# Optimization experiments

Measured on AMD Instinct MI355X. Metric: run time of the kernel, lower is better.

## Reference

```python
import jax, jax.numpy as jnp
import numpy as np
from jax import lax

EPS = 1e-6

def rms_norm(x, w):
    return x * lax.rsqrt(jnp.mean(x * x, axis=-1, keepdims=True) + EPS) * w

def rec_layer(x, conv_w, conv_b, Wr_w, Wr_b, Wi_w, Wi_b, log_a, out_w, norm_w):
    # x: [B, L, d]; depthwise causal conv, kernel size 4
    B, L, d = x.shape
    xc = lax.conv_general_dilated(
        x.transpose(0, 2, 1), conv_w, window_strides=(1,), padding=[(3, 0)],
        dimension_numbers=("NCH", "OIH", "NCH"), feature_group_count=d)
    x_conv = xc.transpose(0, 2, 1) + conv_b  # [B, L, d]
    r_t = jax.nn.sigmoid(x_conv @ Wr_w.T + Wr_b)
    i_t = jax.nn.sigmoid(x_conv @ Wi_w.T + Wi_b)
    a_base = jax.nn.sigmoid(log_a)  # [d]
    a_t = jnp.power(a_base, 8.0 * r_t)  # [B, L, d]
    u_t = i_t * x_conv

    def step(h, au):
        a, u = au
        h = a * h + jnp.sqrt(jnp.clip(1.0 - a * a, 0.0, None)) * u
        return h, h

    _, hs = lax.scan(step, jnp.zeros((B, d), x.dtype),
                     (a_t.transpose(1, 0, 2), u_t.transpose(1, 0, 2)))
    out = hs.transpose(1, 0, 2)  # [B, L, d]
    return rms_norm(out @ out_w.T, norm_w)

def setup_inputs() -> dict:
    B, L, M, d, do = 8, 2048, 256, 1024, 256
    key = jax.random.key(0)
    ks = jax.random.split(key, 24)
    inp = {
        "concept_out": jax.random.normal(ks[0], (B, M, d), jnp.float32),
        "encoder_out": jax.random.normal(ks[1], (B, L, d), jnp.float32),
        "boundary_probs": jax.random.uniform(ks[2], (B, L), jnp.float32),
        "boundary_idx": jnp.sort(jax.random.randint(ks[3], (B, M), 0, L, jnp.int32), axis=1),
        "gate_w": jax.random.normal(ks[4], (d, d), jnp.float32) * 0.02,
        "gate_b": jnp.zeros((d,), jnp.float32),
        "down_w": jax.random.normal(ks[5], (do, d), jnp.float32) * 0.02,
        "up_w": jax.random.normal(ks[6], (d, do), jnp.float32) * 0.02,
        "norm_out_w": jnp.ones((d,), jnp.float32),
        "rec_conv_w": jax.random.normal(ks[7], (3, do, 1, 4), jnp.float32) * 0.02,
        "rec_conv_b": jnp.zeros((3, do), jnp.float32),
        "rec_Wr_w": jax.random.normal(ks[8], (3, do, do), jnp.float32) * 0.02,
        "rec_Wr_b": jnp.zeros((3, do), jnp.float32),
        "rec_Wi_w": jax.random.normal(ks[9], (3, do, do), jnp.float32) * 0.02,
        "rec_Wi_b": jnp.zeros((3, do), jnp.float32),
        "rec_log_a": jnp.full((3, do), 7.5, jnp.float32),
        "rec_out_w": jax.random.normal(ks[10], (3, do, do), jnp.float32) * 0.02,
        "rec_norm_w": jnp.ones((3, do), jnp.float32),
    }
    return inp

def reference(concept_out, encoder_out, boundary_probs, boundary_idx,
              gate_w, gate_b, down_w, up_w, norm_out_w,
              rec_conv_w, rec_conv_b, rec_Wr_w, rec_Wr_b,
              rec_Wi_w, rec_Wi_b, rec_log_a, rec_out_w, rec_norm_w):
    B, L, d = encoder_out.shape
    M = concept_out.shape[1]
    # 1. EMA smoothing over boundaries
    p_at_bounds = jnp.take_along_axis(boundary_probs, boundary_idx, axis=1)  # [B, M]

    def ema_step(h, pc):
        p_i, c_i = pc  # [B], [B, d]
        h = p_i[:, None] * c_i + (1.0 - p_i[:, None]) * h
        return h, h

    _, sm = lax.scan(ema_step, jnp.zeros((B, d), concept_out.dtype),
                     (p_at_bounds.T, concept_out.transpose(1, 0, 2)))
    smoothed = sm.transpose(1, 0, 2)  # [B, M, d]
    # 2. Plug-back via searchsorted (== torch.bucketize right=True)
    arange_L = jnp.arange(L)
    counts = jax.vmap(lambda bi: jnp.searchsorted(bi, arange_L, side="right"))(boundary_idx)
    bucket = jnp.clip(counts - 1, 0, None)  # [B, L]
    plugback = jnp.take_along_axis(smoothed, bucket[..., None], axis=1)  # [B, L, d]
    # 3. Gated residual
    gate = jax.nn.sigmoid(encoder_out @ gate_w.T + gate_b)
    h = (1.0 - boundary_probs[..., None]) * gate * encoder_out + plugback
    # 4. Decoder recurrence
    h = h @ down_w.T
    for k in range(3):
        h = rec_layer(h, rec_conv_w[k], rec_conv_b[k], rec_Wr_w[k], rec_Wr_b[k],
                      rec_Wi_w[k], rec_Wi_b[k], rec_log_a[k], rec_out_w[k], rec_norm_w[k])
    h = h @ up_w.T
    return rms_norm(h, norm_out_w)
```

## Files before the change

kernel.cpp:

```cpp
#include <hip/hip_runtime.h>
#include <hip/hip_bf16.h>
#include <stdint.h>

typedef __attribute__((ext_vector_type(8))) short short8;
typedef __attribute__((ext_vector_type(4))) float f32x4;
typedef __hip_bfloat16 bf16;

#define NB   8
#define LSEQ 2048
#define NM   256
#define DMODEL 1024
#define DO   256
#define BLR  16384
#define NCH  32
#define CLK  64

__device__ __forceinline__ float sigm(float x) { return 1.f / (1.f + __expf(-x)); }

__device__ __forceinline__ void gl_lds16(const void* g, void* l) {
  __builtin_amdgcn_global_load_lds((const __attribute__((address_space(1))) void*)g,
                                   (__attribute__((address_space(3))) void*)l, 16, 0, 0);
}

__device__ __forceinline__ short8 ds_read128(const bf16* p) {
  short8 r;
  unsigned a = (unsigned)(uintptr_t)(const __attribute__((address_space(3))) bf16*)p;
  asm volatile("ds_read_b128 %0, %1" : "=v"(r) : "v"(a));
  return r;
}

__device__ __forceinline__ unsigned short bf16bits(float v) {
  bf16 b = __float2bfloat16(v);
  return *(unsigned short*)&b;
}
__device__ __forceinline__ float bits2f(unsigned short u) {
  bf16 b = *(bf16*)&u;
  return __bfloat162float(b);
}


__global__ __launch_bounds__(256) void prep_kernel(
    const float* __restrict__ gate_w, const float* __restrict__ down_w,
    const float* __restrict__ up_w, const float* __restrict__ wr_w,
    const float* __restrict__ wi_w, const float* __restrict__ ow_w,
    const float* __restrict__ log_a,
    bf16* __restrict__ gate_wb, bf16* __restrict__ down_wb, bf16* __restrict__ up_wb,
    bf16* __restrict__ wrb, bf16* __restrict__ wib, bf16* __restrict__ owb,
    float* __restrict__ e8) {
  int i = blockIdx.x * 256 + threadIdx.x;
  if (i < 1048576) { gate_wb[i] = __float2bfloat16(gate_w[i]); return; }
  i -= 1048576;
  if (i < 262144) { down_wb[i] = __float2bfloat16(down_w[i]); return; }
  i -= 262144;
  if (i < 262144) { up_wb[i] = __float2bfloat16(up_w[i]); return; }
  i -= 262144;
  if (i < 196608) { wrb[i] = __float2bfloat16(wr_w[i]); return; }
  i -= 196608;
  if (i < 196608) { wib[i] = __float2bfloat16(wi_w[i]); return; }
  i -= 196608;
  if (i < 196608) { owb[i] = __float2bfloat16(ow_w[i]); return; }
  i -= 196608;
  if (i < 768) {
    float ab = 1.f / (1.f + expf(-log_a[i]));
    e8[i] = 8.f * log2f(ab);
  }
}

__global__ __launch_bounds__(256) void cvt4_kernel(const float4* __restrict__ in,
                                                   ushort4* __restrict__ out, int n4) {
  int i = blockIdx.x * 256 + threadIdx.x;
  if (i < n4) {
    float4 v = in[i];
    ushort4 o;
    o.x = bf16bits(v.x); o.y = bf16bits(v.y); o.z = bf16bits(v.z); o.w = bf16bits(v.w);
    out[i] = o;
  }
}


__global__ __launch_bounds__(256) void ema_kernel(const float* __restrict__ cpt,
                                                  const float* __restrict__ bprobs,
                                                  const int* __restrict__ bidx,
                                                  float* __restrict__ smoothed) {
  int b = blockIdx.x >> 2;
  int c = ((blockIdx.x & 3) << 8) + threadIdx.x;
  __shared__ float p[NM];
  p[threadIdx.x] = bprobs[b * LSEQ + bidx[b * NM + threadIdx.x]];
  __syncthreads();
  const float* cp = cpt + (size_t)b * NM * DMODEL + c;
  float* sp = smoothed + (size_t)b * NM * DMODEL + c;
  float h = 0.f;
  for (int m = 0; m < NM; ++m) {
    float pm = p[m];
    h = pm * cp[(size_t)m * DMODEL] + (1.f - pm) * h;
    sp[(size_t)m * DMODEL] = h;
  }
}

__global__ __launch_bounds__(256) void bucket_kernel(const int* __restrict__ bidx,
                                                     int* __restrict__ bucket) {
  int i = blockIdx.x * 256 + threadIdx.x;
  int b = i >> 11, l = i & 2047;
  const int* bi = bidx + b * NM;
  int lo = 0, hi = NM;
  while (lo < hi) {
    int mid = (lo + hi) >> 1;
    if (bi[mid] <= l) lo = mid + 1; else hi = mid;
  }
  int v = lo - 1;
  bucket[i] = v < 0 ? 0 : v;
}


__global__ __launch_bounds__(256) void gate_plug_kernel(bf16* __restrict__ h0,
                                                        const bf16* __restrict__ encb,
                                                        const float* __restrict__ gbias,
                                                        const float* __restrict__ bprobs,
                                                        const int* __restrict__ bucket,
                                                        const float* __restrict__ smoothed) {
  const int m = blockIdx.x;
  const int t = threadIdx.x;
  const int b = m >> 11;
  const float pm1 = 1.f - bprobs[m];
  const float* srow = smoothed + ((size_t)(b * NM + bucket[m])) * DMODEL + t * 4;
  const size_t base = (size_t)m * DMODEL + t * 4;
  ushort4 gr = *(const ushort4*)(h0 + base);
  ushort4 er = *(const ushort4*)(encb + base);
  float4 sm4 = *(const float4*)srow;
  float4 gb4 = *(const float4*)(gbias + t * 4);
  ushort4 o;
  o.x = bf16bits(pm1 * sigm(bits2f(gr.x) + gb4.x) * bits2f(er.x) + sm4.x);
  o.y = bf16bits(pm1 * sigm(bits2f(gr.y) + gb4.y) * bits2f(er.y) + sm4.y);
  o.z = bf16bits(pm1 * sigm(bits2f(gr.z) + gb4.z) * bits2f(er.z) + sm4.z);
  o.w = bf16bits(pm1 * sigm(bits2f(gr.w) + gb4.w) * bits2f(er.w) + sm4.w);
  *(ushort4*)(h0 + base) = o;
}


__global__ __launch_bounds__(256) void conv_kernel(const bf16* __restrict__ x,
                                                   const float* __restrict__ cw,
                                                   const float* __restrict__ cb,
                                                   bf16* __restrict__ xcb) {
  int i = blockIdx.x * 256 + threadIdx.x;
  int c = i & 255;
  int bl = i >> 8;
  int l = bl & 2047;
  float4 w4 = ((const float4*)cw)[c];
  const float* wf = (const float*)&w4;
  float s = cb[c];
#pragma unroll
  for (int kk = 0; kk < 4; ++kk) {
    int ll = l - 3 + kk;
    if (ll >= 0) s += wf[kk] * __bfloat162float(x[i + (kk - 3) * 256]);
  }
  xcb[i] = __float2bfloat16(s);
}


__global__ __launch_bounds__(256) void scan_p1(const unsigned int* __restrict__ ds,
                                               float2* __restrict__ AS) {
  int b = blockIdx.x >> 5, ch = blockIdx.x & 31, c = threadIdx.x;
  size_t base = ((size_t)b * LSEQ + ch * CLK) * DO + c;
  float A = 1.f, S = 0.f;
  for (int t = 0; t < CLK; ++t) {
    unsigned int u = ds[base + (size_t)t * DO];
    float d = bits2f((unsigned short)(u & 0xffff));
    float s = bits2f((unsigned short)(u >> 16));
    float a = 1.f - d;
    A *= a;
    S = __builtin_fmaf(a, S, s);
  }
  AS[blockIdx.x * DO + c] = make_float2(A, S);
}

__global__ __launch_bounds__(256) void scan_p2(const unsigned int* __restrict__ ds,
                                               const float2* __restrict__ AS,
                                               bf16* __restrict__ hs) {
  int b = blockIdx.x >> 5, ch = blockIdx.x & 31, c = threadIdx.x;
  float h = 0.f;
  for (int j = 0; j < ch; ++j) {
    float2 as = AS[(b * NCH + j) * DO + c];
    h = __builtin_fmaf(as.x, h, as.y);
  }
  size_t base = ((size_t)b * LSEQ + ch * CLK) * DO + c;
  for (int t = 0; t < CLK; ++t) {
    unsigned int u = ds[base + (size_t)t * DO];
    float d = bits2f((unsigned short)(u & 0xffff));
    float s = bits2f((unsigned short)(u >> 16));
    h = __builtin_fmaf(-d, h, h) + s;
    hs[base + (size_t)t * DO] = __float2bfloat16(h);
  }
}


__global__ __launch_bounds__(256) void rmsnorm1024_kernel(const bf16* __restrict__ in,
                                                          const float* __restrict__ w,
                                                          float* __restrict__ out) {
  int row = blockIdx.x, t = threadIdx.x;
  ushort4 raw = ((const ushort4*)(in + (size_t)row * 1024))[t];
  float v0 = bits2f(raw.x), v1 = bits2f(raw.y), v2 = bits2f(raw.z), v3 = bits2f(raw.w);
  float ss = v0 * v0 + v1 * v1 + v2 * v2 + v3 * v3;
#pragma unroll
  for (int ofs = 32; ofs > 0; ofs >>= 1) ss += __shfl_down(ss, ofs, 64);
  __shared__ float wsum[4];
  if ((t & 63) == 0) wsum[t >> 6] = ss;
  __syncthreads();
  float tot = wsum[0] + wsum[1] + wsum[2] + wsum[3];
  float sc = rsqrtf(tot * (1.f / 1024.f) + 1e-6f);
  float4 wv = ((const float4*)w)[t];
  float4 o;
  o.x = v0 * sc * wv.x; o.y = v1 * sc * wv.y;
  o.z = v2 * sc * wv.z; o.w = v3 * sc * wv.w;
  ((float4*)(out + (size_t)row * 1024))[t] = o;
}


struct EpA {
  bf16* outb;
  const float* bias;
  const bf16* encb;
  const float* p;
  const int* bucket;
  const float* smoothed;
};


template <int EP, int NC, int KC>
__global__ __launch_bounds__(256) void gemm_bt(const bf16* __restrict__ A,
                                               const bf16* __restrict__ W, EpA ep) {
  __shared__ __align__(16) bf16 As[128 * 64];
  __shared__ __align__(16) bf16 Bs[128 * 64];
  const int t = threadIdx.x;
  const int lane = t & 63;
  const int wv = t >> 6;
  const int wm = wv >> 1, wn = wv & 1;
  const int quad = lane >> 4, l16 = lane & 15;
  const int bm = blockIdx.x << 7, bn = blockIdx.y << 7;

  f32x4 acc[4][4] = {};

  for (int k0 = 0; k0 < KC; k0 += 64) {
    __syncthreads();
#pragma unroll
    for (int i = 0; i < 4; ++i) {
      int slot = i * 256 + t;
      int m = slot >> 3;
      int lk8 = (slot & 7) ^ (m & 7);
      gl_lds16(A + (size_t)(bm + m) * KC + k0 + lk8 * 8, As + slot * 8);
      gl_lds16(W + (size_t)(bn + m) * KC + k0 + lk8 * 8, Bs + slot * 8);
    }
    __syncthreads();
#pragma unroll
    for (int ks = 0; ks < 2; ++ks) {
      short8 af[4], bfr[4];
#pragma unroll
      for (int i = 0; i < 4; ++i) {
        int m = wm * 64 + i * 16 + l16;
        int pa = (ks * 4 + quad) ^ (m & 7);
        af[i] = *(const short8*)(As + m * 64 + pa * 8);
        int n = wn * 64 + i * 16 + l16;
        int pb = (ks * 4 + quad) ^ (n & 7);
        bfr[i] = *(const short8*)(Bs + n * 64 + pb * 8);
      }
#pragma unroll
      for (int i = 0; i < 4; ++i)
#pragma unroll
        for (int j = 0; j < 4; ++j)
          acc[i][j] = __builtin_amdgcn_mfma_f32_16x16x32_bf16(af[i], bfr[j], acc[i][j], 0, 0, 0);
    }
  }

#pragma unroll
  for (int i = 0; i < 4; ++i) {
#pragma unroll
    for (int j = 0; j < 4; ++j) {
#pragma unroll
      for (int r = 0; r < 4; ++r) {
        int m = bm + wm * 64 + i * 16 + quad * 4 + r;
        int n = bn + wn * 64 + j * 16 + l16;
        size_t idx = (size_t)m * NC + n;
        float v = acc[i][j][r];
        if (EP == 1) {
          float g = sigm(v + ep.bias[n]);
          float pm = ep.p[m];
          int bb = m >> 11;
          float sm = ep.smoothed[((size_t)(bb * NM + ep.bucket[m])) * DMODEL + n];
          float e = __bfloat162float(ep.encb[idx]);
          ep.outb[idx] = __float2bfloat16((1.f - pm) * g * e + sm);
        } else {
          ep.outb[idx] = __float2bfloat16(v);
        }
      }
    }
  }
}


template <int KC>
__global__ __launch_bounds__(512, 2) void gemm256(const bf16* __restrict__ Ag,
                                                  const bf16* __restrict__ W,
                                                  bf16* __restrict__ outb) {
  __shared__ __align__(16) bf16 lds[2][4][128 * 64];
  const int t = threadIdx.x;
  const int lane = t & 63;
  const int wv = t >> 6;
  const int wm = wv >> 2, wn = wv & 3;
  const int quad = lane >> 4, l16 = lane & 15;
  const int bm = blockIdx.x << 8, bn = blockIdx.y << 8;
  constexpr int KT = KC >> 6;
  constexpr int KM = KT - 1;

  const int rr = t >> 3;
  const int cc = (t & 7) ^ (rr & 7);

  f32x4 acc[8][4] = {};
  short8 af[4][2], bfr[2][2];

#define STAGE_A(BUF, H, KTI)                                                      \
  {                                                                               \
    int kk = ((KTI) & KM) << 6;                                                   \
    const bf16* s0 = Ag + (size_t)(bm + (H) * 64 + rr) * KC + kk + cc * 8;        \
    gl_lds16(s0, &lds[BUF][H][t * 8]);                                            \
    const bf16* s1 = Ag + (size_t)(bm + (H) * 64 + rr + 128) * KC + kk + cc * 8;  \
    gl_lds16(s1, &lds[BUF][H][(512 + t) * 8]);                                    \
  }
#define STAGE_B(BUF, H, KTI)                                                      \
  {                                                                               \
    int kk = ((KTI) & KM) << 6;                                                   \
    int n0 = (H) * 32 + (rr & 31) + ((rr >> 5) << 6);                             \
    const bf16* s0 = W + (size_t)(bn + n0) * KC + kk + cc * 8;                    \
    gl_lds16(s0, &lds[BUF][2 + (H)][t * 8]);                                      \
    const bf16* s1 = W + (size_t)(bn + n0 + 128) * KC + kk + cc * 8;              \
    gl_lds16(s1, &lds[BUF][2 + (H)][(512 + t) * 8]);                              \
  }
#define LD_A(BUF, MG)                                                             \
  _Pragma("unroll") for (int ii = 0; ii < 4; ++ii) {                              \
    int r = wm * 64 + ii * 16 + l16;                                              \
    _Pragma("unroll") for (int ks = 0; ks < 2; ++ks) {                            \
      int ch = (ks * 4 + quad) ^ (r & 7);                                         \
      af[ii][ks] = ds_read128(&lds[BUF][MG][(r * 8 + ch) * 8]);                   \
    }                                                                             \
  }
#define LD_B(BUF, NG)                                                             \
  _Pragma("unroll") for (int jj = 0; jj < 2; ++jj) {                              \
    int r = wn * 32 + jj * 16 + l16;                                              \
    _Pragma("unroll") for (int ks = 0; ks < 2; ++ks) {                            \
      int ch = (ks * 4 + quad) ^ (r & 7);                                         \
      bfr[jj][ks] = ds_read128(&lds[BUF][2 + (NG)][(r * 8 + ch) * 8]);            \
    }                                                                             \
  }
#define MMA(MG, NG)                                                               \
  _Pragma("unroll") for (int ks = 0; ks < 2; ++ks)                                \
  _Pragma("unroll") for (int ii = 0; ii < 4; ++ii)                                \
  _Pragma("unroll") for (int jj = 0; jj < 2; ++jj)                                \
    acc[(MG) * 4 + ii][(NG) * 2 + jj] = __builtin_amdgcn_mfma_f32_16x16x32_bf16(  \
        af[ii][ks], bfr[jj][ks], acc[(MG) * 4 + ii][(NG) * 2 + jj], 0, 0, 0);
#define BARR __builtin_amdgcn_s_barrier()
#define WAIT_LGKM asm volatile("s_waitcnt lgkmcnt(0)" ::: "memory")
#define WAIT_VM6 asm volatile("s_waitcnt vmcnt(6)" ::: "memory")
#define SBAR __builtin_amdgcn_sched_barrier(0)
#define PH(MG, NG)                   \
  BARR; WAIT_LGKM; SBAR;             \
  __builtin_amdgcn_s_setprio(1);     \
  MMA(MG, NG);                       \
  __builtin_amdgcn_s_setprio(0);     \
  SBAR;                              \
  BARR;
#define PH_V(MG, NG)                 \
  BARR; WAIT_LGKM; SBAR;             \
  __builtin_amdgcn_s_setprio(1);     \
  MMA(MG, NG);                       \
  __builtin_amdgcn_s_setprio(0);     \
  SBAR;                              \
  WAIT_VM6;                          \
  BARR;

  STAGE_A(0, 0, 0) STAGE_A(0, 1, 0) STAGE_B(0, 0, 0) STAGE_B(0, 1, 0)
  STAGE_A(1, 0, 1) STAGE_A(1, 1, 1) STAGE_B(1, 1, 1)
  WAIT_VM6;
  BARR;

#pragma unroll 1
  for (int it = 0; it < (KT >> 1); ++it) {
    const int kt = it * 2;
    LD_A(0, 0) LD_B(0, 0)
    STAGE_B(1, 0, kt + 1)
    PH(0, 0)
    LD_B(0, 1)
    STAGE_A(0, 0, kt + 2)
    PH(0, 1)
    LD_A(0, 1)
    STAGE_B(0, 1, kt + 2)
    PH(1, 1)
    LD_B(0, 0)
    STAGE_A(0, 1, kt + 2)
    PH_V(1, 0)
    LD_A(1, 0) LD_B(1, 0)
    STAGE_B(0, 0, kt + 2)
    PH(0, 0)
    LD_B(1, 1)
    STAGE_A(1, 0, kt + 3)
    PH(0, 1)
    LD_A(1, 1)
    STAGE_B(1, 1, kt + 3)
    PH(1, 1)
    LD_B(1, 0)
    STAGE_A(1, 1, kt + 3)
    PH_V(1, 0)
  }

#undef STAGE_A
#undef STAGE_B
#undef LD_A
#undef LD_B
#undef MMA
#undef BARR
#undef WAIT_LGKM
#undef WAIT_VM6
#undef SBAR
#undef PH
#undef PH_V

#pragma unroll
  for (int i = 0; i < 8; ++i) {
#pragma unroll
    for (int j = 0; j < 4; ++j) {
#pragma unroll
      for (int r = 0; r < 4; ++r) {
        int m = bm + wm * 128 + i * 16 + quad * 4 + r;
        int n = bn + wn * 64 + j * 16 + l16;
        outb[(size_t)m * DMODEL + n] = __float2bfloat16(acc[i][j][r]);
      }
    }
  }
}


__global__ __launch_bounds__(256, 4) void gemm_ri(const bf16* __restrict__ A,
                                                  const bf16* __restrict__ Wr,
                                                  const bf16* __restrict__ Wi,
                                                  const float* __restrict__ rbias,
                                                  const float* __restrict__ ibias,
                                                  const float* __restrict__ e8,
                                                  unsigned int* __restrict__ ds_out) {
  __shared__ __align__(16) bf16 As[32 * 64];
  __shared__ __align__(16) bf16 Br[128 * 64];
  __shared__ __align__(16) bf16 Bi[128 * 64];
  const int t = threadIdx.x;
  const int lane = t & 63;
  const int wv = t >> 6;
  const int wm = wv >> 1, wn = wv & 1;
  const int quad = lane >> 4, l16 = lane & 15;
  const int bm = blockIdx.x << 5;
  const int bn = blockIdx.y << 7;

  f32x4 ar[4] = {};
  f32x4 ai[4] = {};

  for (int k0 = 0; k0 < DO; k0 += 64) {
    __syncthreads();
    {
      int m = t >> 3, lk8 = (t & 7) ^ (m & 7);
      gl_lds16(A + (size_t)(bm + m) * DO + k0 + lk8 * 8, As + t * 8);
    }
#pragma unroll
    for (int i = 0; i < 4; ++i) {
      int slot = i * 256 + t;
      int n = slot >> 3, lk8 = (slot & 7) ^ (n & 7);
      gl_lds16(Wr + (size_t)(bn + n) * DO + k0 + lk8 * 8, Br + slot * 8);
      gl_lds16(Wi + (size_t)(bn + n) * DO + k0 + lk8 * 8, Bi + slot * 8);
    }
    __syncthreads();
#pragma unroll
    for (int ks = 0; ks < 2; ++ks) {
      int m = wm * 16 + l16;
      int pa = (ks * 4 + quad) ^ (m & 7);
      short8 af = *(const short8*)(As + m * 64 + pa * 8);
#pragma unroll
      for (int j = 0; j < 4; ++j) {
        int n = wn * 64 + j * 16 + l16;
        int pb = (ks * 4 + quad) ^ (n & 7);
        short8 br = *(const short8*)(Br + n * 64 + pb * 8);
        short8 bi = *(const short8*)(Bi + n * 64 + pb * 8);
        ar[j] = __builtin_amdgcn_mfma_f32_16x16x32_bf16(af, br, ar[j], 0, 0, 0);
        ai[j] = __builtin_amdgcn_mfma_f32_16x16x32_bf16(af, bi, ai[j], 0, 0, 0);
      }
    }
  }

#pragma unroll
  for (int j = 0; j < 4; ++j) {
    int n = bn + wn * 64 + j * 16 + l16;
    float rb = rbias[n], ib = ibias[n], e8n = e8[n];
#pragma unroll
    for (int r = 0; r < 4; ++r) {
      int m = bm + wm * 16 + quad * 4 + r;
      size_t idx = (size_t)m * DO + n;
      float rv = sigm(ar[j][r] + rb);
      float a = exp2f(rv * e8n);
      float d = 1.f - a;
      float iv = sigm(ai[j][r] + ib);
      float xc = __bfloat162float(A[idx]);
      float s = sqrtf(fmaxf(1.f - a * a, 0.f)) * iv * xc;
      ds_out[idx] = (unsigned int)bf16bits(d) | ((unsigned int)bf16bits(s) << 16);
    }
  }
}


__global__ __launch_bounds__(256) void gemm_on(const bf16* __restrict__ A,
                                               const bf16* __restrict__ W,
                                               const float* __restrict__ rnw,
                                               bf16* __restrict__ xb) {
  __shared__ __align__(16) bf16 As[64 * 64];
  __shared__ __align__(16) bf16 Bs[256 * 64];
  __shared__ float red[4][64];
  const int t = threadIdx.x;
  const int lane = t & 63;
  const int wn = t >> 6;
  const int quad = lane >> 4, l16 = lane & 15;
  const int bm = blockIdx.x << 6;

  f32x4 acc[4][4] = {};

  for (int k0 = 0; k0 < DO; k0 += 64) {
    __syncthreads();
#pragma unroll
    for (int i = 0; i < 2; ++i) {
      int slot = i * 256 + t;
      int m = slot >> 3;
      int lk8 = (slot & 7) ^ (m & 7);
      gl_lds16(A + (size_t)(bm + m) * DO + k0 + lk8 * 8, As + slot * 8);
    }
#pragma unroll
    for (int i = 0; i < 8; ++i) {
      int slot = i * 256 + t;
      int n = slot >> 3;
      int lk8 = (slot & 7) ^ (n & 7);
      gl_lds16(W + (size_t)n * DO + k0 + lk8 * 8, Bs + slot * 8);
    }
    __syncthreads();
#pragma unroll
    for (int ks = 0; ks < 2; ++ks) {
      short8 af[4], bfr[4];
#pragma unroll
      for (int i = 0; i < 4; ++i) {
        int m = i * 16 + l16;
        int pa = (ks * 4 + quad) ^ (m & 7);
        af[i] = *(const short8*)(As + m * 64 + pa * 8);
        int n = wn * 64 + i * 16 + l16;
        int pb = (ks * 4 + quad) ^ (n & 7);
        bfr[i] = *(const short8*)(Bs + n * 64 + pb * 8);
      }
#pragma unroll
      for (int i = 0; i < 4; ++i)
#pragma unroll
        for (int j = 0; j < 4; ++j)
          acc[i][j] = __builtin_amdgcn_mfma_f32_16x16x32_bf16(af[i], bfr[j], acc[i][j], 0, 0, 0);
    }
  }

  float part[4][4];
#pragma unroll
  for (int i = 0; i < 4; ++i)
#pragma unroll
    for (int r = 0; r < 4; ++r) {
      float s = 0.f;
#pragma unroll
      for (int j = 0; j < 4; ++j) s += acc[i][j][r] * acc[i][j][r];
      part[i][r] = s;
    }
#pragma unroll
  for (int mask = 1; mask <= 8; mask <<= 1)
#pragma unroll
    for (int i = 0; i < 4; ++i)
#pragma unroll
      for (int r = 0; r < 4; ++r) part[i][r] += __shfl_xor(part[i][r], mask, 64);
  if (l16 == 0) {
#pragma unroll
    for (int i = 0; i < 4; ++i)
#pragma unroll
      for (int r = 0; r < 4; ++r) red[wn][i * 16 + quad * 4 + r] = part[i][r];
  }
  __syncthreads();
#pragma unroll
  for (int i = 0; i < 4; ++i) {
#pragma unroll
    for (int r = 0; r < 4; ++r) {
      int ml = i * 16 + quad * 4 + r;
      float tot = red[0][ml] + red[1][ml] + red[2][ml] + red[3][ml];
      float sc = rsqrtf(tot * (1.f / 256.f) + 1e-6f);
#pragma unroll
      for (int j = 0; j < 4; ++j) {
        int n = wn * 64 + j * 16 + l16;
        xb[(size_t)(bm + ml) * DO + n] = __float2bfloat16(acc[i][j][r] * sc * rnw[n]);
      }
    }
  }
}


extern "C" void kernel_launch(void* const* d_in, const int* in_sizes, int n_in,
                              void* d_out, int out_size, void* d_ws, size_t ws_size,
                              hipStream_t stream) {
  const float* concept_out = (const float*)d_in[0];
  const float* encoder_out = (const float*)d_in[1];
  const float* bprobs      = (const float*)d_in[2];
  const int*   bidx        = (const int*)d_in[3];
  const float* gate_w      = (const float*)d_in[4];
  const float* gate_b      = (const float*)d_in[5];
  const float* down_w      = (const float*)d_in[6];
  const float* up_w        = (const float*)d_in[7];
  const float* norm_out_w  = (const float*)d_in[8];
  const float* rc_w        = (const float*)d_in[9];
  const float* rc_b        = (const float*)d_in[10];
  const float* wr_w        = (const float*)d_in[11];
  const float* wr_b        = (const float*)d_in[12];
  const float* wi_w        = (const float*)d_in[13];
  const float* wi_b        = (const float*)d_in[14];
  const float* log_a       = (const float*)d_in[15];
  const float* ow_w        = (const float*)d_in[16];
  const float* rn_w        = (const float*)d_in[17];
  float* out = (float*)d_out;
  (void)in_sizes; (void)n_in; (void)out_size; (void)ws_size;

  char* base = (char*)d_ws;
  size_t off = 0;
  auto alloc = [&](size_t bytes) -> char* {
    char* p = base + off;
    off += (bytes + 255) & ~(size_t)255;
    return p;
  };
  float* smoothed = (float*)alloc((size_t)NB * NM * DMODEL * 4);
  int*   bucket   = (int*)alloc((size_t)BLR * 4);
  bf16*  gate_wb  = (bf16*)alloc((size_t)DMODEL * DMODEL * 2);
  bf16*  down_wb  = (bf16*)alloc((size_t)DO * DMODEL * 2);
  bf16*  up_wb    = (bf16*)alloc((size_t)DMODEL * DO * 2);
  bf16*  wrb      = (bf16*)alloc((size_t)3 * DO * DO * 2);
  bf16*  wib      = (bf16*)alloc((size_t)3 * DO * DO * 2);
  bf16*  owb      = (bf16*)alloc((size_t)3 * DO * DO * 2);
  float* e8       = (float*)alloc(3 * DO * 4);
  float2* ASsum   = (float2*)alloc((size_t)NB * NCH * DO * 8);
  bf16*  xb       = (bf16*)alloc((size_t)BLR * DO * 2);

  const size_t SZ_ENC   = (size_t)BLR * DMODEL * 2;
  const size_t SZ_XCONV = (size_t)BLR * DO * 2;
  const size_t SZ_DS    = (size_t)BLR * DO * 4;
  char* RA = alloc(2 * SZ_ENC);
  bf16*  encb = (bf16*)RA;
  bf16*  h0b  = (bf16*)(RA + SZ_ENC);
  bf16*         xconvb = (bf16*)RA;
  unsigned int* dsbuf  = (unsigned int*)(RA + SZ_XCONV);
  bf16*         hsb    = (bf16*)(RA + SZ_XCONV + SZ_DS);
  bf16*  tmp2b  = (bf16*)RA;

  cvt4_kernel<<<(BLR * DMODEL / 4 + 255) / 256, 256, 0, stream>>>(
      (const float4*)encoder_out, (ushort4*)encb, BLR * DMODEL / 4);
  prep_kernel<<<(2163456 + 255) / 256, 256, 0, stream>>>(
      gate_w, down_w, up_w, wr_w, wi_w, ow_w, log_a,
      gate_wb, down_wb, up_wb, wrb, wib, owb, e8);
  ema_kernel<<<NB * 4, 256, 0, stream>>>(concept_out, bprobs, bidx, smoothed);
  bucket_kernel<<<BLR / 256, 256, 0, stream>>>(bidx, bucket);

  gemm256<DMODEL><<<dim3(BLR / 256, DMODEL / 256), 512, 0, stream>>>(encb, gate_wb, h0b);
  gate_plug_kernel<<<BLR, 256, 0, stream>>>(h0b, encb, gate_b, bprobs, bucket, smoothed);

  EpA ep{};
  ep.outb = xb;
  gemm_bt<5, DO, DMODEL><<<dim3(BLR / 128, DO / 128), 256, 0, stream>>>(h0b, down_wb, ep);

  for (int k = 0; k < 3; ++k) {
    conv_kernel<<<BLR, 256, 0, stream>>>(xb, rc_w + k * DO * 4, rc_b + k * DO, xconvb);
    gemm_ri<<<dim3(BLR / 32, DO / 128), 256, 0, stream>>>(
        xconvb, wrb + k * DO * DO, wib + k * DO * DO,
        wr_b + k * DO, wi_b + k * DO, e8 + k * DO, dsbuf);
    scan_p1<<<NB * NCH, 256, 0, stream>>>(dsbuf, ASsum);
    scan_p2<<<NB * NCH, 256, 0, stream>>>(dsbuf, ASsum, hsb);
    gemm_on<<<BLR / 64, 256, 0, stream>>>(hsb, owb + k * DO * DO, rn_w + k * DO, xb);
  }

  gemm256<DO><<<dim3(BLR / 256, DMODEL / 256), 512, 0, stream>>>(xb, up_wb, tmp2b);
  rmsnorm1024_kernel<<<BLR, 256, 0, stream>>>(tmp2b, norm_out_w, out);
}
```

Before: 486.4 us.

## Merge prep/convert and ema/bucket launches, shrink GEMM tiles, vectorize conv

The encoder fp32-to-bf16 conversion moves into prep_kernel, and the EMA and bucket kernels become one launch, which removes two kernel launches. The down-projection GEMM becomes a dedicated 64x128-tile kernel, and gemm_on's tile drops from 64 to 32 rows. Both GEMMs now set launch_bounds for 4 blocks per CU, giving more blocks and higher occupancy. The depthwise conv processes four channels per thread with vector loads and stores, at the cost of less reuse per tile in the GEMMs.

```diff
diff --git a/kernel.cpp b/kernel.cpp
--- a/kernel.cpp
+++ b/kernel.cpp
@@ -40,6 +40,7 @@
 
 
 __global__ __launch_bounds__(256) void prep_kernel(
+    const float* __restrict__ encoder_out, ushort4* __restrict__ encb4,
     const float* __restrict__ gate_w, const float* __restrict__ down_w,
     const float* __restrict__ up_w, const float* __restrict__ wr_w,
     const float* __restrict__ wi_w, const float* __restrict__ ow_w,
@@ -48,6 +49,14 @@
     bf16* __restrict__ wrb, bf16* __restrict__ wib, bf16* __restrict__ owb,
     float* __restrict__ e8) {
   int i = blockIdx.x * 256 + threadIdx.x;
+  if (i < 4194304) {
+    float4 v = ((const float4*)encoder_out)[i];
+    ushort4 o;
+    o.x = bf16bits(v.x); o.y = bf16bits(v.y); o.z = bf16bits(v.z); o.w = bf16bits(v.w);
+    encb4[i] = o;
+    return;
+  }
+  i -= 4194304;
   if (i < 1048576) { gate_wb[i] = __float2bfloat16(gate_w[i]); return; }
   i -= 1048576;
   if (i < 262144) { down_wb[i] = __float2bfloat16(down_w[i]); return; }
@@ -66,49 +75,38 @@
   }
 }
 
-__global__ __launch_bounds__(256) void cvt4_kernel(const float4* __restrict__ in,
-                                                   ushort4* __restrict__ out, int n4) {
-  int i = blockIdx.x * 256 + threadIdx.x;
-  if (i < n4) {
-    float4 v = in[i];
-    ushort4 o;
-    o.x = bf16bits(v.x); o.y = bf16bits(v.y); o.z = bf16bits(v.z); o.w = bf16bits(v.w);
-    out[i] = o;
-  }
-}
-
-
-__global__ __launch_bounds__(256) void ema_kernel(const float* __restrict__ cpt,
-                                                  const float* __restrict__ bprobs,
-                                                  const int* __restrict__ bidx,
-                                                  float* __restrict__ smoothed) {
-  int b = blockIdx.x >> 2;
-  int c = ((blockIdx.x & 3) << 8) + threadIdx.x;
-  __shared__ float p[NM];
-  p[threadIdx.x] = bprobs[b * LSEQ + bidx[b * NM + threadIdx.x]];
-  __syncthreads();
-  const float* cp = cpt + (size_t)b * NM * DMODEL + c;
-  float* sp = smoothed + (size_t)b * NM * DMODEL + c;
-  float h = 0.f;
-  for (int m = 0; m < NM; ++m) {
-    float pm = p[m];
-    h = pm * cp[(size_t)m * DMODEL] + (1.f - pm) * h;
-    sp[(size_t)m * DMODEL] = h;
-  }
-}
-
-__global__ __launch_bounds__(256) void bucket_kernel(const int* __restrict__ bidx,
-                                                     int* __restrict__ bucket) {
-  int i = blockIdx.x * 256 + threadIdx.x;
-  int b = i >> 11, l = i & 2047;
-  const int* bi = bidx + b * NM;
-  int lo = 0, hi = NM;
-  while (lo < hi) {
-    int mid = (lo + hi) >> 1;
-    if (bi[mid] <= l) lo = mid + 1; else hi = mid;
-  }
-  int v = lo - 1;
-  bucket[i] = v < 0 ? 0 : v;
+
+__global__ __launch_bounds__(256) void ema_bucket_kernel(const float* __restrict__ cpt,
+                                                         const float* __restrict__ bprobs,
+                                                         const int* __restrict__ bidx,
+                                                         float* __restrict__ smoothed,
+                                                         int* __restrict__ bucket) {
+  if (blockIdx.x < NB * 4) {
+    int b = blockIdx.x >> 2;
+    int c = ((blockIdx.x & 3) << 8) + threadIdx.x;
+    __shared__ float p[NM];
+    p[threadIdx.x] = bprobs[b * LSEQ + bidx[b * NM + threadIdx.x]];
+    __syncthreads();
+    const float* cp = cpt + (size_t)b * NM * DMODEL + c;
+    float* sp = smoothed + (size_t)b * NM * DMODEL + c;
+    float h = 0.f;
+    for (int m = 0; m < NM; ++m) {
+      float pm = p[m];
+      h = pm * cp[(size_t)m * DMODEL] + (1.f - pm) * h;
+      sp[(size_t)m * DMODEL] = h;
+    }
+  } else {
+    int i = (blockIdx.x - NB * 4) * 256 + threadIdx.x;
+    int b = i >> 11, l = i & 2047;
+    const int* bi = bidx + b * NM;
+    int lo = 0, hi = NM;
+    while (lo < hi) {
+      int mid = (lo + hi) >> 1;
+      if (bi[mid] <= l) lo = mid + 1; else hi = mid;
+    }
+    int v = lo - 1;
+    bucket[i] = v < 0 ? 0 : v;
+  }
 }
 
 
@@ -141,19 +139,33 @@
                                                    const float* __restrict__ cw,
                                                    const float* __restrict__ cb,
                                                    bf16* __restrict__ xcb) {
-  int i = blockIdx.x * 256 + threadIdx.x;
-  int c = i & 255;
-  int bl = i >> 8;
+  int i4 = blockIdx.x * 256 + threadIdx.x;
+  int cg = i4 & 63;
+  int bl = i4 >> 6;
   int l = bl & 2047;
-  float4 w4 = ((const float4*)cw)[c];
-  const float* wf = (const float*)&w4;
-  float s = cb[c];
+  int c0 = cg << 2;
+  float wf[4][4];
+#pragma unroll
+  for (int cc = 0; cc < 4; ++cc) {
+    float4 w4 = ((const float4*)cw)[c0 + cc];
+    wf[cc][0] = w4.x; wf[cc][1] = w4.y; wf[cc][2] = w4.z; wf[cc][3] = w4.w;
+  }
+  float4 cb4 = *(const float4*)(cb + c0);
+  float s0 = cb4.x, s1 = cb4.y, s2 = cb4.z, s3 = cb4.w;
 #pragma unroll
   for (int kk = 0; kk < 4; ++kk) {
     int ll = l - 3 + kk;
-    if (ll >= 0) s += wf[kk] * __bfloat162float(x[i + (kk - 3) * 256]);
-  }
-  xcb[i] = __float2bfloat16(s);
+    if (ll >= 0) {
+      ushort4 xv = *(const ushort4*)(x + (size_t)(bl + kk - 3) * DO + c0);
+      s0 += wf[0][kk] * bits2f(xv.x);
+      s1 += wf[1][kk] * bits2f(xv.y);
+      s2 += wf[2][kk] * bits2f(xv.z);
+      s3 += wf[3][kk] * bits2f(xv.w);
+    }
+  }
+  ushort4 o;
+  o.x = bf16bits(s0); o.y = bf16bits(s1); o.z = bf16bits(s2); o.w = bf16bits(s3);
+  *(ushort4*)(xcb + (size_t)bl * DO + c0) = o;
 }
 
 
@@ -215,55 +227,52 @@
 }
 
 
-struct EpA {
-  bf16* outb;
-  const float* bias;
-  const bf16* encb;
-  const float* p;
-  const int* bucket;
-  const float* smoothed;
-};
-
-
-template <int EP, int NC, int KC>
-__global__ __launch_bounds__(256) void gemm_bt(const bf16* __restrict__ A,
-                                               const bf16* __restrict__ W, EpA ep) {
-  __shared__ __align__(16) bf16 As[128 * 64];
+__global__ __launch_bounds__(256, 4) void gemm_dn(const bf16* __restrict__ A,
+                                                  const bf16* __restrict__ W,
+                                                  bf16* __restrict__ outb) {
+  __shared__ __align__(16) bf16 As[64 * 64];
   __shared__ __align__(16) bf16 Bs[128 * 64];
   const int t = threadIdx.x;
   const int lane = t & 63;
   const int wv = t >> 6;
   const int wm = wv >> 1, wn = wv & 1;
   const int quad = lane >> 4, l16 = lane & 15;
-  const int bm = blockIdx.x << 7, bn = blockIdx.y << 7;
-
-  f32x4 acc[4][4] = {};
-
-  for (int k0 = 0; k0 < KC; k0 += 64) {
+  const int bm = blockIdx.x << 6, bn = blockIdx.y << 7;
+
+  f32x4 acc[2][4] = {};
+
+  for (int k0 = 0; k0 < DMODEL; k0 += 64) {
     __syncthreads();
+#pragma unroll
+    for (int i = 0; i < 2; ++i) {
+      int slot = i * 256 + t;
+      int m = slot >> 3, lk8 = (slot & 7) ^ (m & 7);
+      gl_lds16(A + (size_t)(bm + m) * DMODEL + k0 + lk8 * 8, As + slot * 8);
+    }
 #pragma unroll
     for (int i = 0; i < 4; ++i) {
       int slot = i * 256 + t;
-      int m = slot >> 3;
-      int lk8 = (slot & 7) ^ (m & 7);
-      gl_lds16(A + (size_t)(bm + m) * KC + k0 + lk8 * 8, As + slot * 8);
-      gl_lds16(W + (size_t)(bn + m) * KC + k0 + lk8 * 8, Bs + slot * 8);
+      int n = slot >> 3, lk8 = (slot & 7) ^ (n & 7);
+      gl_lds16(W + (size_t)(bn + n) * DMODEL + k0 + lk8 * 8, Bs + slot * 8);
     }
     __syncthreads();
 #pragma unroll
     for (int ks = 0; ks < 2; ++ks) {
-      short8 af[4], bfr[4];
-#pragma unroll
-      for (int i = 0; i < 4; ++i) {
-        int m = wm * 64 + i * 16 + l16;
+      short8 af[2], bfr[4];
+#pragma unroll
+      for (int i = 0; i < 2; ++i) {
+        int m = wm * 32 + i * 16 + l16;
         int pa = (ks * 4 + quad) ^ (m & 7);
         af[i] = *(const short8*)(As + m * 64 + pa * 8);
-        int n = wn * 64 + i * 16 + l16;
+      }
+#pragma unroll
+      for (int j = 0; j < 4; ++j) {
+        int n = wn * 64 + j * 16 + l16;
         int pb = (ks * 4 + quad) ^ (n & 7);
-        bfr[i] = *(const short8*)(Bs + n * 64 + pb * 8);
-      }
-#pragma unroll
-      for (int i = 0; i < 4; ++i)
+        bfr[j] = *(const short8*)(Bs + n * 64 + pb * 8);
+      }
+#pragma unroll
+      for (int i = 0; i < 2; ++i)
 #pragma unroll
         for (int j = 0; j < 4; ++j)
           acc[i][j] = __builtin_amdgcn_mfma_f32_16x16x32_bf16(af[i], bfr[j], acc[i][j], 0, 0, 0);
@@ -271,28 +280,15 @@
   }
 
 #pragma unroll
-  for (int i = 0; i < 4; ++i) {
-#pragma unroll
-    for (int j = 0; j < 4; ++j) {
+  for (int i = 0; i < 2; ++i)
+#pragma unroll
+    for (int j = 0; j < 4; ++j)
 #pragma unroll
       for (int r = 0; r < 4; ++r) {
-        int m = bm + wm * 64 + i * 16 + quad * 4 + r;
+        int m = bm + wm * 32 + i * 16 + quad * 4 + r;
         int n = bn + wn * 64 + j * 16 + l16;
-        size_t idx = (size_t)m * NC + n;
-        float v = acc[i][j][r];
-        if (EP == 1) {
-          float g = sigm(v + ep.bias[n]);
-          float pm = ep.p[m];
-          int bb = m >> 11;
-          float sm = ep.smoothed[((size_t)(bb * NM + ep.bucket[m])) * DMODEL + n];
-          float e = __bfloat162float(ep.encb[idx]);
-          ep.outb[idx] = __float2bfloat16((1.f - pm) * g * e + sm);
-        } else {
-          ep.outb[idx] = __float2bfloat16(v);
-        }
-      }
-    }
-  }
+        outb[(size_t)m * DO + n] = __float2bfloat16(acc[i][j][r]);
+      }
 }
 
 
@@ -508,61 +504,60 @@
 }
 
 
-__global__ __launch_bounds__(256) void gemm_on(const bf16* __restrict__ A,
-                                               const bf16* __restrict__ W,
-                                               const float* __restrict__ rnw,
-                                               bf16* __restrict__ xb) {
-  __shared__ __align__(16) bf16 As[64 * 64];
+__global__ __launch_bounds__(256, 4) void gemm_on(const bf16* __restrict__ A,
+                                                  const bf16* __restrict__ W,
+                                                  const float* __restrict__ rnw,
+                                                  bf16* __restrict__ xb) {
+  __shared__ __align__(16) bf16 As[32 * 64];
   __shared__ __align__(16) bf16 Bs[256 * 64];
-  __shared__ float red[4][64];
+  __shared__ float red[4][32];
   const int t = threadIdx.x;
   const int lane = t & 63;
   const int wn = t >> 6;
   const int quad = lane >> 4, l16 = lane & 15;
-  const int bm = blockIdx.x << 6;
-
-  f32x4 acc[4][4] = {};
+  const int bm = blockIdx.x << 5;
+
+  f32x4 acc[2][4] = {};
 
   for (int k0 = 0; k0 < DO; k0 += 64) {
     __syncthreads();
-#pragma unroll
-    for (int i = 0; i < 2; ++i) {
-      int slot = i * 256 + t;
-      int m = slot >> 3;
-      int lk8 = (slot & 7) ^ (m & 7);
-      gl_lds16(A + (size_t)(bm + m) * DO + k0 + lk8 * 8, As + slot * 8);
+    {
+      int m = t >> 3, lk8 = (t & 7) ^ (m & 7);
+      gl_lds16(A + (size_t)(bm + m) * DO + k0 + lk8 * 8, As + t * 8);
     }
 #pragma unroll
     for (int i = 0; i < 8; ++i) {
       int slot = i * 256 + t;
-      int n = slot >> 3;
-      int lk8 = (slot & 7) ^ (n & 7);
+      int n = slot >> 3, lk8 = (slot & 7) ^ (n & 7);
       gl_lds16(W + (size_t)n * DO + k0 + lk8 * 8, Bs + slot * 8);
     }
     __syncthreads();
 #pragma unroll
     for (int ks = 0; ks < 2; ++ks) {
-      short8 af[4], bfr[4];
-#pragma unroll
-      for (int i = 0; i < 4; ++i) {
+      short8 af[2], bfr[4];
+#pragma unroll
+      for (int i = 0; i < 2; ++i) {
         int m = i * 16 + l16;
         int pa = (ks * 4 + quad) ^ (m & 7);
         af[i] = *(const short8*)(As + m * 64 + pa * 8);
-        int n = wn * 64 + i * 16 + l16;
+      }
+#pragma unroll
+      for (int j = 0; j < 4; ++j) {
+        int n = wn * 64 + j * 16 + l16;
         int pb = (ks * 4 + quad) ^ (n & 7);
-        bfr[i] = *(const short8*)(Bs + n * 64 + pb * 8);
-      }
-#pragma unroll
-      for (int i = 0; i < 4; ++i)
+        bfr[j] = *(const short8*)(Bs + n * 64 + pb * 8);
+      }
+#pragma unroll
+      for (int i = 0; i < 2; ++i)
 #pragma unroll
         for (int j = 0; j < 4; ++j)
           acc[i][j] = __builtin_amdgcn_mfma_f32_16x16x32_bf16(af[i], bfr[j], acc[i][j], 0, 0, 0);
     }
   }
 
-  float part[4][4];
-#pragma unroll
-  for (int i = 0; i < 4; ++i)
+  float part[2][4];
+#pragma unroll
+  for (int i = 0; i < 2; ++i)
 #pragma unroll
     for (int r = 0; r < 4; ++r) {
       float s = 0.f;
@@ -573,18 +568,18 @@
 #pragma unroll
   for (int mask = 1; mask <= 8; mask <<= 1)
 #pragma unroll
-    for (int i = 0; i < 4; ++i)
+    for (int i = 0; i < 2; ++i)
 #pragma unroll
       for (int r = 0; r < 4; ++r) part[i][r] += __shfl_xor(part[i][r], mask, 64);
   if (l16 == 0) {
 #pragma unroll
-    for (int i = 0; i < 4; ++i)
+    for (int i = 0; i < 2; ++i)
 #pragma unroll
       for (int r = 0; r < 4; ++r) red[wn][i * 16 + quad * 4 + r] = part[i][r];
   }
   __syncthreads();
 #pragma unroll
-  for (int i = 0; i < 4; ++i) {
+  for (int i = 0; i < 2; ++i) {
 #pragma unroll
     for (int r = 0; r < 4; ++r) {
       int ml = i * 16 + quad * 4 + r;
@@ -654,29 +649,26 @@
   bf16*         hsb    = (bf16*)(RA + SZ_XCONV + SZ_DS);
   bf16*  tmp2b  = (bf16*)RA;
 
-  cvt4_kernel<<<(BLR * DMODEL / 4 + 255) / 256, 256, 0, stream>>>(
-      (const float4*)encoder_out, (ushort4*)encb, BLR * DMODEL / 4);
-  prep_kernel<<<(2163456 + 255) / 256, 256, 0, stream>>>(
+  prep_kernel<<<(4194304 + 2163456 + 255) / 256, 256, 0, stream>>>(
+      encoder_out, (ushort4*)encb,
       gate_w, down_w, up_w, wr_w, wi_w, ow_w, log_a,
       gate_wb, down_wb, up_wb, wrb, wib, owb, e8);
-  ema_kernel<<<NB * 4, 256, 0, stream>>>(concept_out, bprobs, bidx, smoothed);
-  bucket_kernel<<<BLR / 256, 256, 0, stream>>>(bidx, bucket);
+  ema_bucket_kernel<<<NB * 4 + BLR / 256, 256, 0, stream>>>(
+      concept_out, bprobs, bidx, smoothed, bucket);
 
   gemm256<DMODEL><<<dim3(BLR / 256, DMODEL / 256), 512, 0, stream>>>(encb, gate_wb, h0b);
   gate_plug_kernel<<<BLR, 256, 0, stream>>>(h0b, encb, gate_b, bprobs, bucket, smoothed);
 
-  EpA ep{};
-  ep.outb = xb;
-  gemm_bt<5, DO, DMODEL><<<dim3(BLR / 128, DO / 128), 256, 0, stream>>>(h0b, down_wb, ep);
+  gemm_dn<<<dim3(BLR / 64, DO / 128), 256, 0, stream>>>(h0b, down_wb, xb);
 
   for (int k = 0; k < 3; ++k) {
-    conv_kernel<<<BLR, 256, 0, stream>>>(xb, rc_w + k * DO * 4, rc_b + k * DO, xconvb);
+    conv_kernel<<<BLR * 64 / 256, 256, 0, stream>>>(xb, rc_w + k * DO * 4, rc_b + k * DO, xconvb);
     gemm_ri<<<dim3(BLR / 32, DO / 128), 256, 0, stream>>>(
         xconvb, wrb + k * DO * DO, wib + k * DO * DO,
         wr_b + k * DO, wi_b + k * DO, e8 + k * DO, dsbuf);
     scan_p1<<<NB * NCH, 256, 0, stream>>>(dsbuf, ASsum);
     scan_p2<<<NB * NCH, 256, 0, stream>>>(dsbuf, ASsum, hsb);
-    gemm_on<<<BLR / 64, 256, 0, stream>>>(hsb, owb + k * DO * DO, rn_w + k * DO, xb);
+    gemm_on<<<BLR / 32, 256, 0, stream>>>(hsb, owb + k * DO * DO, rn_w + k * DO, xb);
   }
 
   gemm256<DO><<<dim3(BLR / 256, DMODEL / 256), 512, 0, stream>>>(xb, up_wb, tmp2b);
```

Measured after the change: 472.2 us. 2.9% less time.
